# Kernel tuning notes

Hardware: AMD Instinct MI355X
Metric: run time of the kernel (lower is better)

Reference implementation:

```python
import jax, jax.numpy as jnp
import numpy as np

N = 50000
E = 800000
IN_DIM = 128
OUT_DIM = 128
HEADS = 4
HEAD_DIM = OUT_DIM // HEADS  # 32


def setup_inputs() -> dict:
    key = jax.random.key(0)
    k1, k2, k3, k4 = jax.random.split(key, 4)
    x = jax.random.normal(k1, (N, IN_DIM), dtype=jnp.float32)
    edge_index = jax.random.randint(k2, (2, E), 0, N, dtype=jnp.int32)
    # nn.Linear(in_dim, out_dim): weight [out_dim, in_dim]
    W = jax.random.normal(k3, (OUT_DIM, IN_DIM), dtype=jnp.float32) * (1.0 / np.sqrt(IN_DIM))
    # nn.Linear(2*head_dim, 1): weight [1, 2*head_dim] -> flattened [2*head_dim]
    a_w = jax.random.normal(k4, (2 * HEAD_DIM,), dtype=jnp.float32) * (1.0 / np.sqrt(2 * HEAD_DIM))
    return {"x": x, "edge_index": edge_index, "W": W, "a_w": a_w}


def reference(x, edge_index, W, a_w):
    n = x.shape[0]
    Wx = (x @ W.T).reshape(n, HEADS, HEAD_DIM)          # [N,H,D]
    src, dst = edge_index[0], edge_index[1]
    Wx_src = Wx[src]                                     # [E,H,D]
    Wx_dst = Wx[dst]                                     # [E,H,D]
    # a([Wx_src || Wx_dst]) = Wx_src @ a_src + Wx_dst @ a_dst
    a_src, a_dst = a_w[:HEAD_DIM], a_w[HEAD_DIM:]
    e = jnp.einsum('ehd,d->eh', Wx_src, a_src) + jnp.einsum('ehd,d->eh', Wx_dst, a_dst)
    e = jax.nn.leaky_relu(e, negative_slope=0.2)         # [E,H]
    # numerically-stable segment softmax over incoming edges of each dst node
    e_max = jax.ops.segment_max(e, dst, num_segments=n)  # [N,H], -inf for empty
    e_exp = jnp.exp(e - e_max[dst])                      # [E,H]
    denom = jax.ops.segment_sum(e_exp, dst, num_segments=n)  # [N,H]
    alpha = e_exp / (denom[dst] + 1e-8)                  # [E,H] (dropout=0 -> identity)
    weighted = alpha[..., None] * Wx_src                 # [E,H,D]
    out = jax.ops.segment_sum(weighted, dst, num_segments=n)  # [N,H,D]
    return jax.nn.elu(out.reshape(n, OUT_DIM))
```

## Files before the change

### kernel.cpp

```cpp
#include <hip/hip_runtime.h>
#include <hip/hip_bf16.h>
#include <math.h>

#define HEADS 4
#define NBKT 196
#define CAPB 4608

typedef short bf16x8 __attribute__((ext_vector_type(8)));
typedef float f32x4 __attribute__((ext_vector_type(4)));
typedef unsigned short ushort8 __attribute__((ext_vector_type(8)));

__device__ __forceinline__ float lrelu(float v) { return v >= 0.f ? v : 0.2f * v; }

__device__ __forceinline__ unsigned short f2bf(float f) {
    unsigned u = __float_as_uint(f);
    return (unsigned short)((u + 0x7FFF + ((u >> 16) & 1)) >> 16);
}

__device__ __forceinline__ unsigned pk2bf(float a, float b) {
    __hip_bfloat162 h = __float22bfloat162_rn(make_float2(a, b));
    unsigned u;
    __builtin_memcpy(&u, &h, 4);
    return u;
}

__global__ __launch_bounds__(256, 2) void fused_kernel(const float* __restrict__ x,
                                                       const float* __restrict__ W,
                                                       const float* __restrict__ aw,
                                                       const int* __restrict__ ei,
                                                       unsigned short* __restrict__ Wxh,
                                                       float* __restrict__ s_src,
                                                       float* __restrict__ s_dst,
                                                       int* __restrict__ gcur,
                                                       unsigned* __restrict__ gbuf,
                                                       int n, int E, int ngemm) {
    __shared__ __align__(16) char smem[66304];
    const int t = threadIdx.x;

    if ((int)blockIdx.x < ngemm) {
        unsigned short* Alds = (unsigned short*)smem;
        unsigned short* Blds = (unsigned short*)(smem + 32768);
        float* sawm = (float*)(smem + 65536);
        const int w = t >> 6, l = t & 63;
        const int q = l >> 4, l16 = l & 15;
        const int node0 = blockIdx.x * 128;

        if (t < 64) sawm[t] = aw[t];

#pragma unroll
        for (int i = 0; i < 8; ++i) {
            int c = i * 256 + t;
            int nl = c >> 4, k8 = c & 15;
            int gn = node0 + nl;
            if (gn >= n) gn = n - 1;
            const float4* gp = (const float4*)(x + (size_t)gn * 128 + k8 * 8);
            float4 v0 = gp[0], v1 = gp[1];
            uint4 u = make_uint4(pk2bf(v0.x, v0.y), pk2bf(v0.z, v0.w),
                                 pk2bf(v1.x, v1.y), pk2bf(v1.z, v1.w));
            int ch = (((nl >> 4) * 4 + (k8 >> 2)) * 4 + (k8 & 3)) * 16 + (nl & 15);
            *(uint4*)(&Alds[ch * 8]) = u;
        }
#pragma unroll
        for (int i = 0; i < 8; ++i) {
            int c = i * 256 + t;
            int dl = c >> 4, k8 = c & 15;
            const float4* gp = (const float4*)(W + (size_t)dl * 128 + k8 * 8);
            float4 v0 = gp[0], v1 = gp[1];
            uint4 u = make_uint4(pk2bf(v0.x, v0.y), pk2bf(v0.z, v0.w),
                                 pk2bf(v1.x, v1.y), pk2bf(v1.z, v1.w));
            int ch = (((dl >> 4) * 4 + (k8 >> 2)) * 4 + (k8 & 3)) * 16 + (dl & 15);
            *(uint4*)(&Blds[ch * 8]) = u;
        }
        __syncthreads();

        f32x4 acc[2][8];
#pragma unroll
        for (int rt = 0; rt < 2; ++rt)
#pragma unroll
            for (int ct = 0; ct < 8; ++ct) acc[rt][ct] = (f32x4){0.f, 0.f, 0.f, 0.f};

#pragma unroll
        for (int kk = 0; kk < 4; ++kk) {
            bf16x8 a0 = *(const bf16x8*)(&Alds[(((w * 2 + 0) * 4 + kk) * 64 + l) * 8]);
            bf16x8 a1 = *(const bf16x8*)(&Alds[(((w * 2 + 1) * 4 + kk) * 64 + l) * 8]);
#pragma unroll
            for (int ct = 0; ct < 8; ++ct) {
                bf16x8 b = *(const bf16x8*)(&Blds[((ct * 4 + kk) * 64 + l) * 8]);
                acc[0][ct] = __builtin_amdgcn_mfma_f32_16x16x32_bf16(a0, b, acc[0][ct], 0, 0, 0);
                acc[1][ct] = __builtin_amdgcn_mfma_f32_16x16x32_bf16(a1, b, acc[1][ct], 0, 0, 0);
            }
        }

        __syncthreads();
#pragma unroll
        for (int rt = 0; rt < 2; ++rt) {
            int nl = w * 32 + rt * 16 + q * 4;
#pragma unroll
            for (int ct = 0; ct < 8; ++ct) {
                int dim = ct * 16 + l16;
                Alds[(nl + 0) * 128 + dim] = f2bf(acc[rt][ct][0]);
                Alds[(nl + 1) * 128 + dim] = f2bf(acc[rt][ct][1]);
                Alds[(nl + 2) * 128 + dim] = f2bf(acc[rt][ct][2]);
                Alds[(nl + 3) * 128 + dim] = f2bf(acc[rt][ct][3]);
            }
        }
        __syncthreads();

#pragma unroll
        for (int i = 0; i < 8; ++i) {
            int c = i * 256 + t;
            int nl = c >> 4, d8 = c & 15;
            int gn = node0 + nl;
            ushort8 u = *(const ushort8*)(&Alds[nl * 128 + d8 * 8]);
            if (gn < n) *(ushort8*)(Wxh + (size_t)gn * 128 + d8 * 8) = u;
            float sp = 0.f, dp = 0.f;
            int ab = (d8 & 3) * 8;
#pragma unroll
            for (int j = 0; j < 8; ++j) {
                float v = __uint_as_float(((unsigned)(unsigned short)u[j]) << 16);
                sp += v * sawm[ab + j];
                dp += v * sawm[32 + ab + j];
            }
            sp += __shfl_xor(sp, 1, 64); dp += __shfl_xor(dp, 1, 64);
            sp += __shfl_xor(sp, 2, 64); dp += __shfl_xor(dp, 2, 64);
            if ((l & 3) == 0 && gn < n) {
                int h = (l & 15) >> 2;
                s_src[(size_t)gn * 4 + h] = sp;
                s_dst[(size_t)gn * 4 + h] = dp;
            }
        }
    } else {
        int* hist = (int*)smem;
        int* scanws = (int*)(smem + 1024);
        int* lbase = (int*)(smem + 2048);
        int* lcur = (int*)(smem + 3072);
        int* gb = (int*)(smem + 4096);
        unsigned* sorted = (unsigned*)(smem + 5120);
        unsigned char* bkt = (unsigned char*)(smem + 21504);

        const int blk = blockIdx.x - ngemm;
        const int b0 = blk * 4096;
        const int total = min(4096, E - b0);

        hist[t] = 0;
        __syncthreads();

        unsigned pk[16];
#pragma unroll
        for (int i = 0; i < 16; ++i) {
            int idx = i * 256 + t;
            if (idx < total) {
                int e = b0 + idx;
                unsigned s = (unsigned)ei[e], d = (unsigned)ei[E + e];
                pk[i] = s | (d << 16);
                atomicAdd(&hist[d >> 8], 1);
            }
        }
        __syncthreads();
        int v = hist[t];
        scanws[t] = v;
        __syncthreads();
        for (int off = 1; off < 256; off <<= 1) {
            int y = (t >= off) ? scanws[t - off] : 0;
            __syncthreads();
            scanws[t] += y;
            __syncthreads();
        }
        int ex = scanws[t] - v;
        lbase[t] = ex;
        lcur[t] = ex;
        if (t < NBKT) gb[t] = (v > 0) ? atomicAdd(&gcur[t], v) : 0;
        __syncthreads();
#pragma unroll
        for (int i = 0; i < 16; ++i) {
            int idx = i * 256 + t;
            if (idx < total) {
                int b = pk[i] >> 24;
                int qpos = atomicAdd(&lcur[b], 1);
                sorted[qpos] = pk[i];
                bkt[qpos] = (unsigned char)b;
            }
        }
        __syncthreads();
#pragma unroll
        for (int i = 0; i < 16; ++i) {
            int s = i * 256 + t;
            if (s < total) {
                int b = bkt[s];
                int pos = gb[b] + (s - lbase[b]);
                if (pos < CAPB) gbuf[(size_t)b * CAPB + pos] = sorted[s];
            }
        }
    }
}

__global__ __launch_bounds__(256) void pass2_kernel(const int* __restrict__ gcur,
                                                    const unsigned* __restrict__ gbuf,
                                                    unsigned short* __restrict__ csr,
                                                    int2* __restrict__ node_info, int n) {
    __shared__ int hist[256], scanws[256], cur[256];
    const int t = threadIdx.x;
    const int bucket = blockIdx.x;
    int cnt = gcur[bucket];
    if (cnt > CAPB) cnt = CAPB;
    const unsigned* gp = gbuf + (size_t)bucket * CAPB;

    hist[t] = 0;
    __syncthreads();

    unsigned e[18];
#pragma unroll
    for (int i = 0; i < 18; ++i) {
        int idx = i * 256 + t;
        if (idx < cnt) {
            e[i] = gp[idx];
            atomicAdd(&hist[(e[i] >> 16) & 255], 1);
        }
    }
    __syncthreads();
    int v = hist[t];
    scanws[t] = v;
    __syncthreads();
    for (int off = 1; off < 256; off <<= 1) {
        int y = (t >= off) ? scanws[t - off] : 0;
        __syncthreads();
        scanws[t] += y;
        __syncthreads();
    }
    int ex = scanws[t] - v;
    cur[t] = ex;
    int node = bucket * 256 + t;
    if (node < n) node_info[node] = make_int2(bucket * CAPB + ex, v);
    __syncthreads();
#pragma unroll
    for (int i = 0; i < 18; ++i) {
        int idx = i * 256 + t;
        if (idx < cnt) {
            int ld = (e[i] >> 16) & 255;
            int qpos = atomicAdd(&cur[ld], 1);
            csr[(size_t)bucket * CAPB + qpos] = (unsigned short)(e[i] & 0xFFFF);
        }
    }
}

__global__ __launch_bounds__(256) void accum_kernel(const int2* __restrict__ node_info,
                                                    const unsigned short* __restrict__ csr,
                                                    const float* __restrict__ s_src,
                                                    const float* __restrict__ s_dst,
                                                    const unsigned short* __restrict__ Wxh,
                                                    float* __restrict__ out, int n) {
    int wid = threadIdx.x >> 6, lane = threadIdx.x & 63;
    int node = blockIdx.x * 4 + wid;
    if (node >= n) return;
    int l = lane & 15, grp = lane >> 4;
    int h = l >> 2;
    int2 info = node_info[node];
    int start = info.x, deg = info.y;
    float sdn = s_dst[(size_t)node * 4 + h];

    float acc[8] = {0.f, 0.f, 0.f, 0.f, 0.f, 0.f, 0.f, 0.f};
    float dsum = 0.f;
    for (int i = grp; i < deg; i += 8) {
        int i1 = i + 4;
        bool has1 = i1 < deg;
        int src0 = csr[start + i];
        int src1 = has1 ? csr[start + i1] : src0;
        float w0 = __expf(lrelu(s_src[(size_t)src0 * 4 + h] + sdn));
        float w1 = has1 ? __expf(lrelu(s_src[(size_t)src1 * 4 + h] + sdn)) : 0.f;
        ushort8 u0 = *(const ushort8*)(Wxh + (size_t)src0 * 128 + l * 8);
        ushort8 u1 = *(const ushort8*)(Wxh + (size_t)src1 * 128 + l * 8);
        dsum += w0 + w1;
#pragma unroll
        for (int j = 0; j < 8; ++j) {
            float v0 = __uint_as_float(((unsigned)(unsigned short)u0[j]) << 16);
            float v1 = __uint_as_float(((unsigned)(unsigned short)u1[j]) << 16);
            acc[j] += w0 * v0 + w1 * v1;
        }
    }
#pragma unroll
    for (int m = 16; m <= 32; m <<= 1) {
#pragma unroll
        for (int j = 0; j < 8; ++j) acc[j] += __shfl_xor(acc[j], m, 64);
        dsum += __shfl_xor(dsum, m, 64);
    }
    if (grp == 0) {
        float inv = 1.f / (dsum + 1e-8f);
        float o[8];
#pragma unroll
        for (int j = 0; j < 8; ++j) {
            float v = acc[j] * inv;
            o[j] = v > 0.f ? v : expm1f(v);
        }
        float4* dp = (float4*)(out + (size_t)node * 128 + l * 8);
        dp[0] = make_float4(o[0], o[1], o[2], o[3]);
        dp[1] = make_float4(o[4], o[5], o[6], o[7]);
    }
}

extern "C" void kernel_launch(void* const* d_in, const int* in_sizes, int n_in,
                              void* d_out, int out_size, void* d_ws, size_t ws_size,
                              hipStream_t stream) {
    const float* x = (const float*)d_in[0];
    const int* ei = (const int*)d_in[1];
    const float* W = (const float*)d_in[2];
    const float* aw = (const float*)d_in[3];
    float* out = (float*)d_out;
    const int n = in_sizes[0] / 128;
    const int E = in_sizes[1] / 2;

    char* ws = (char*)d_ws;
    size_t off = 0;
    unsigned short* Wxh = (unsigned short*)(ws + off); off += (size_t)n * 128 * 2;
    float* s_src = (float*)(ws + off);     off += (size_t)n * HEADS * 4;
    float* s_dst = (float*)(ws + off);     off += (size_t)n * HEADS * 4;
    int* gcur = (int*)(ws + off);          off += 1024;
    unsigned* gbuf = (unsigned*)(ws + off); off += (size_t)NBKT * CAPB * 4;
    unsigned short* csr = (unsigned short*)(ws + off); off += (size_t)NBKT * CAPB * 2;
    int2* node_info = (int2*)(ws + off);   off += (size_t)n * 8;

    const int ngemm = (n + 127) / 128;
    const int npass1 = (E + 4095) / 4096;

    hipMemsetAsync(gcur, 0, 1024, stream);
    fused_kernel<<<ngemm + npass1, 256, 0, stream>>>(x, W, aw, ei, Wxh, s_src, s_dst,
                                                     gcur, gbuf, n, E, ngemm);
    pass2_kernel<<<npass1, 256, 0, stream>>>(gcur, gbuf, csr, node_info, n);
    accum_kernel<<<(n + 3) / 4, 256, 0, stream>>>(node_info, csr, s_src, s_dst, Wxh, out, n);
}
```

Measured before the change: 150.1 us.

## Pad CSR rows to multiples of 8 with sentinel node and use bf16 dot2 accumulation

Each node's CSR segment is padded to a multiple of 8 and the padding is filled with a sentinel source node whose score is -1e30, so its softmax weight underflows to zero. This lets the accumulation loop drop its bounds checks and conditional second edge. The inner loop packs the two edge weights into bf16 and uses v_dot2_f32_bf16 with byte permutes to accumulate two edges per instruction, replacing the per-element unpack and FMA. Risks: the weights lose precision by being rounded to bf16, the sentinel row of Wxh is never written (harmless only while its weight stays exactly zero), and the padding adds extra gathers.

```diff
diff --git a/kernel.cpp b/kernel.cpp
--- a/kernel.cpp
+++ b/kernel.cpp
@@ -5,6 +5,7 @@
 #define HEADS 4
 #define NBKT 196
 #define CAPB 4608
+#define CAPP 6656
 
 typedef short bf16x8 __attribute__((ext_vector_type(8)));
 typedef float f32x4 __attribute__((ext_vector_type(4)));
@@ -197,7 +198,8 @@
 __global__ __launch_bounds__(256) void pass2_kernel(const int* __restrict__ gcur,
                                                     const unsigned* __restrict__ gbuf,
                                                     unsigned short* __restrict__ csr,
-                                                    int2* __restrict__ node_info, int n) {
+                                                    int2* __restrict__ node_info,
+                                                    float* __restrict__ s_src, int n) {
     __shared__ int hist[256], scanws[256], cur[256];
     const int t = threadIdx.x;
     const int bucket = blockIdx.x;
@@ -205,6 +207,8 @@
     if (cnt > CAPB) cnt = CAPB;
     const unsigned* gp = gbuf + (size_t)bucket * CAPB;
 
+    if (bucket == 0 && t < 4) s_src[(size_t)n * 4 + t] = -1e30f;
+
     hist[t] = 0;
     __syncthreads();
 
@@ -219,7 +223,8 @@
     }
     __syncthreads();
     int v = hist[t];
-    scanws[t] = v;
+    int vp = (v + 7) & ~7;
+    scanws[t] = vp;
     __syncthreads();
     for (int off = 1; off < 256; off <<= 1) {
         int y = (t >= off) ? scanws[t - off] : 0;
@@ -227,10 +232,11 @@
         scanws[t] += y;
         __syncthreads();
     }
-    int ex = scanws[t] - v;
+    int ex = scanws[t] - vp;
     cur[t] = ex;
     int node = bucket * 256 + t;
-    if (node < n) node_info[node] = make_int2(bucket * CAPB + ex, v);
+    if (node < n) node_info[node] = make_int2(bucket * CAPP + ex, vp);
+    for (int j = v; j < vp; ++j) csr[(size_t)bucket * CAPP + ex + j] = (unsigned short)n;
     __syncthreads();
 #pragma unroll
     for (int i = 0; i < 18; ++i) {
@@ -238,7 +244,7 @@
         if (idx < cnt) {
             int ld = (e[i] >> 16) & 255;
             int qpos = atomicAdd(&cur[ld], 1);
-            csr[(size_t)bucket * CAPB + qpos] = (unsigned short)(e[i] & 0xFFFF);
+            csr[(size_t)bucket * CAPP + qpos] = (unsigned short)(e[i] & 0xFFFF);
         }
     }
 }
@@ -257,24 +263,27 @@
     int2 info = node_info[node];
     int start = info.x, deg = info.y;
     float sdn = s_dst[(size_t)node * 4 + h];
+    const unsigned ONE2 = 0x3F803F80u;
 
     float acc[8] = {0.f, 0.f, 0.f, 0.f, 0.f, 0.f, 0.f, 0.f};
     float dsum = 0.f;
     for (int i = grp; i < deg; i += 8) {
-        int i1 = i + 4;
-        bool has1 = i1 < deg;
         int src0 = csr[start + i];
-        int src1 = has1 ? csr[start + i1] : src0;
-        float w0 = __expf(lrelu(s_src[(size_t)src0 * 4 + h] + sdn));
-        float w1 = has1 ? __expf(lrelu(s_src[(size_t)src1 * 4 + h] + sdn)) : 0.f;
-        ushort8 u0 = *(const ushort8*)(Wxh + (size_t)src0 * 128 + l * 8);
-        ushort8 u1 = *(const ushort8*)(Wxh + (size_t)src1 * 128 + l * 8);
-        dsum += w0 + w1;
-#pragma unroll
-        for (int j = 0; j < 8; ++j) {
-            float v0 = __uint_as_float(((unsigned)(unsigned short)u0[j]) << 16);
-            float v1 = __uint_as_float(((unsigned)(unsigned short)u1[j]) << 16);
-            acc[j] += w0 * v0 + w1 * v1;
+        int src1 = csr[start + i + 4];
+        uint4 U0 = *(const uint4*)(Wxh + ((size_t)src0 << 7) + l * 8);
+        uint4 U1 = *(const uint4*)(Wxh + ((size_t)src1 << 7) + l * 8);
+        float w0 = __expf(lrelu(s_src[src0 * 4 + h] + sdn));
+        float w1 = __expf(lrelu(s_src[src1 * 4 + h] + sdn));
+        unsigned wp = pk2bf(w0, w1);
+        asm("v_dot2_f32_bf16 %0, %1, %2, %0" : "+v"(dsum) : "v"(wp), "v"(ONE2));
+        unsigned uu0[4] = {U0.x, U0.y, U0.z, U0.w};
+        unsigned uu1[4] = {U1.x, U1.y, U1.z, U1.w};
+#pragma unroll
+        for (int j = 0; j < 4; ++j) {
+            unsigned lo = __builtin_amdgcn_perm(uu0[j], uu1[j], 0x01000504u);
+            unsigned hi = __builtin_amdgcn_perm(uu0[j], uu1[j], 0x03020706u);
+            asm("v_dot2_f32_bf16 %0, %1, %2, %0" : "+v"(acc[2 * j]) : "v"(wp), "v"(lo));
+            asm("v_dot2_f32_bf16 %0, %1, %2, %0" : "+v"(acc[2 * j + 1]) : "v"(wp), "v"(hi));
         }
     }
 #pragma unroll
@@ -310,12 +319,12 @@
 
     char* ws = (char*)d_ws;
     size_t off = 0;
-    unsigned short* Wxh = (unsigned short*)(ws + off); off += (size_t)n * 128 * 2;
-    float* s_src = (float*)(ws + off);     off += (size_t)n * HEADS * 4;
+    unsigned short* Wxh = (unsigned short*)(ws + off); off += (size_t)(n + 8) * 128 * 2;
+    float* s_src = (float*)(ws + off);     off += (size_t)(n + 1) * HEADS * 4;
     float* s_dst = (float*)(ws + off);     off += (size_t)n * HEADS * 4;
     int* gcur = (int*)(ws + off);          off += 1024;
     unsigned* gbuf = (unsigned*)(ws + off); off += (size_t)NBKT * CAPB * 4;
-    unsigned short* csr = (unsigned short*)(ws + off); off += (size_t)NBKT * CAPB * 2;
+    unsigned short* csr = (unsigned short*)(ws + off); off += (size_t)NBKT * CAPP * 2;
     int2* node_info = (int2*)(ws + off);   off += (size_t)n * 8;
 
     const int ngemm = (n + 127) / 128;
@@ -324,6 +333,6 @@
     hipMemsetAsync(gcur, 0, 1024, stream);
     fused_kernel<<<ngemm + npass1, 256, 0, stream>>>(x, W, aw, ei, Wxh, s_src, s_dst,
                                                      gcur, gbuf, n, E, ngemm);
-    pass2_kernel<<<npass1, 256, 0, stream>>>(gcur, gbuf, csr, node_info, n);
+    pass2_kernel<<<npass1, 256, 0, stream>>>(gcur, gbuf, csr, node_info, s_src, n);
     accum_kernel<<<(n + 3) / 4, 256, 0, stream>>>(node_info, csr, s_src, s_dst, Wxh, out, n);
 }
```

Result: faster. 144.2 us (-3.9%).
